# Kernel tuning notes

Measured on AMD Instinct MI355X. Metric: run time of the kernel, lower is better.

The kernel has to match this reference:

```python
import jax, jax.numpy as jnp
import numpy as np

B, T, C = 4, 1024, 2048
H, HKV, HD = 32, 8, 64
HID = 5632  # round_up(8*2048/3, 256)
EPS = 1e-6


def rmsnorm(x, scale):
    return x * scale * jax.lax.rsqrt(jnp.mean(x * x, axis=-1, keepdims=True) + EPS)


def rotary(t, cos, sin):
    # interleaved even/odd rotation, matching torch apply_rotary_emb
    te, to = t[..., ::2], t[..., 1::2]
    return jnp.stack((te * cos - to * sin, te * sin + to * cos), axis=-1).reshape(t.shape)


def setup_inputs() -> dict:
    key = jax.random.key(0)
    ks = jax.random.split(key, 8)
    s = 0.02
    inv = 1.0 / (10000.0 ** (np.arange(0, HD, 2, dtype=np.float64) / HD))
    ang = np.arange(T, dtype=np.float64)[:, None] * inv[None, :]
    return {
        "x": jax.random.normal(ks[0], (B, T, C), jnp.float32),
        "cos": jnp.asarray(np.cos(ang), jnp.float32),
        "sin": jnp.asarray(np.sin(ang), jnp.float32),
        "w_attn": jax.random.normal(ks[1], (C, (H + 2 * HKV) * HD), jnp.float32) * s,
        "w_proj": jax.random.normal(ks[2], (C, C), jnp.float32) * s,
        "w_gate": jax.random.normal(ks[3], (C, HID), jnp.float32) * s,
        "w_up": jax.random.normal(ks[4], (C, HID), jnp.float32) * s,
        "w_down": jax.random.normal(ks[5], (HID, C), jnp.float32) * s,
        "scale1": jnp.ones((C,), jnp.float32),
        "scale2": jnp.ones((C,), jnp.float32),
    }


def reference(x, cos, sin, w_attn, w_proj, w_gate, w_up, w_down, scale1, scale2):
    n_rep = H // HKV
    # --- attention block ---
    h = rmsnorm(x, scale1)
    qkv = h @ w_attn  # [B,T,(H+2*HKV)*HD]
    q, k, v = jnp.split(qkv, [H * HD, (H + HKV) * HD], axis=-1)
    q = q.reshape(B, T, H, HD).transpose(0, 2, 1, 3)      # [B,H,T,HD]
    k = k.reshape(B, T, HKV, HD).transpose(0, 2, 1, 3)    # [B,HKV,T,HD]
    v = v.reshape(B, T, HKV, HD).transpose(0, 2, 1, 3)
    q = rotary(q, cos, sin)
    k = rotary(k, cos, sin)
    # GQA: group q heads over kv heads instead of repeat_interleave
    qg = q.reshape(B, HKV, n_rep, T, HD)
    scores = jnp.einsum('bgrtd,bgsd->bgrts', qg, k) / jnp.sqrt(jnp.float32(HD))
    causal = jnp.tril(jnp.ones((T, T), bool))
    scores = jnp.where(causal, scores, jnp.finfo(scores.dtype).min)
    p = jax.nn.softmax(scores, axis=-1)
    y = jnp.einsum('bgrts,bgsd->bgrtd', p, v)
    y = y.reshape(B, H, T, HD).transpose(0, 2, 1, 3).reshape(B, T, C)
    x = x + y @ w_proj
    # --- SwiGLU MLP block ---
    h2 = rmsnorm(x, scale2)
    x = x + (jax.nn.silu(h2 @ w_gate) * (h2 @ w_up)) @ w_down
    return x
```

## Files before the change

### kernel.cpp

```cpp
#include <hip/hip_runtime.h>
#include <stdint.h>

#define B_ 4
#define T_ 1024
#define C_ 2048
#define H_ 32
#define HKV_ 8
#define HD_ 64
#define HID_ 5632

typedef __attribute__((ext_vector_type(8))) short short8;
typedef __attribute__((ext_vector_type(4))) float floatx4;

__device__ __forceinline__ float b2f(short s) {
  unsigned u = ((unsigned)(unsigned short)s) << 16;
  return __uint_as_float(u);
}
__device__ __forceinline__ short f2b(float f) {
  unsigned u = __float_as_uint(f);
  u = u + 0x7fffu + ((u >> 16) & 1u);
  return (short)(u >> 16);
}
__device__ __forceinline__ unsigned pk2(float a, float b) {
  return ((unsigned)(unsigned short)f2b(a)) |
         ((unsigned)(unsigned short)f2b(b) << 16);
}

#define GL2LDS(gp, lp)                                              \
  __builtin_amdgcn_global_load_lds(                                 \
      (const __attribute__((address_space(1))) void*)(gp),          \
      (__attribute__((address_space(3))) void*)(lp), 16, 0, 0)

__global__ __launch_bounds__(256) void convt_kernel(
    const float* __restrict__ W, short* __restrict__ Wt, int K, int N) {
  __shared__ unsigned u[32][65];
  int n0 = blockIdx.x * 64, k0 = blockIdx.y * 64;
  int tx = threadIdx.x & 63, ty = threadIdx.x >> 6;
#pragma unroll
  for (int j = 0; j < 8; ++j) {
    int kpair = ty * 8 + j;
    float lo = W[(size_t)(k0 + 2 * kpair) * N + n0 + tx];
    float hi = W[(size_t)(k0 + 2 * kpair + 1) * N + n0 + tx];
    u[kpair][tx] = pk2(lo, hi);
  }
  __syncthreads();
  int ny = threadIdx.x >> 2, kx = threadIdx.x & 3;
  unsigned vals[8];
#pragma unroll
  for (int i = 0; i < 8; ++i) vals[i] = u[kx * 8 + i][ny];
  uint4* dst = (uint4*)(Wt + (size_t)(n0 + ny) * K + k0 + kx * 16);
  dst[0] = make_uint4(vals[0], vals[1], vals[2], vals[3]);
  dst[1] = make_uint4(vals[4], vals[5], vals[6], vals[7]);
}

__global__ __launch_bounds__(256) void vt_kernel(
    const short* __restrict__ vin, short* __restrict__ vout) {
  __shared__ short t[32][33];
  int t0 = blockIdx.x * 32, d0 = blockIdx.y * 32, bg = blockIdx.z;
  int tx = threadIdx.x & 31, ty = threadIdx.x >> 5;
  const short* src = vin + (size_t)bg * T_ * HD_;
  short* dst = vout + (size_t)bg * T_ * HD_;
#pragma unroll
  for (int j = 0; j < 4; ++j)
    t[ty + j * 8][tx] = src[(size_t)(t0 + ty + j * 8) * HD_ + d0 + tx];
  __syncthreads();
#pragma unroll
  for (int j = 0; j < 4; ++j)
    dst[(size_t)(d0 + ty + j * 8) * T_ + t0 + tx] = t[tx][ty + j * 8];
}

__global__ __launch_bounds__(256) void rmsnorm_kernel(
    const float* __restrict__ x, const float* __restrict__ scale,
    short* __restrict__ out) {
  int row = blockIdx.x, tid = threadIdx.x;
  const float4* xr = (const float4*)(x + (size_t)row * C_);
  float4 v0 = xr[tid], v1 = xr[tid + 256];
  float s = v0.x * v0.x + v0.y * v0.y + v0.z * v0.z + v0.w * v0.w +
            v1.x * v1.x + v1.y * v1.y + v1.z * v1.z + v1.w * v1.w;
  for (int off = 32; off > 0; off >>= 1) s += __shfl_down(s, off, 64);
  __shared__ float red[4];
  if ((tid & 63) == 0) red[tid >> 6] = s;
  __syncthreads();
  float tot = red[0] + red[1] + red[2] + red[3];
  float r = rsqrtf(tot * (1.0f / (float)C_) + 1e-6f);
  const float4* sc = (const float4*)scale;
  float4 s0 = sc[tid], s1 = sc[tid + 256];
  short* o = out + (size_t)row * C_;
  o[tid * 4 + 0] = f2b(v0.x * s0.x * r);
  o[tid * 4 + 1] = f2b(v0.y * s0.y * r);
  o[tid * 4 + 2] = f2b(v0.z * s0.z * r);
  o[tid * 4 + 3] = f2b(v0.w * s0.w * r);
  o[1024 + tid * 4 + 0] = f2b(v1.x * s1.x * r);
  o[1024 + tid * 4 + 1] = f2b(v1.y * s1.y * r);
  o[1024 + tid * 4 + 2] = f2b(v1.z * s1.z * r);
  o[1024 + tid * 4 + 3] = f2b(v1.w * s1.w * r);
}

template <int EPI>
__global__ __launch_bounds__(256, 2) void gemm128_kernel(
    const short* __restrict__ A, const short* __restrict__ Bt,
    void* __restrict__ Out, const float* __restrict__ resid,
    int M, int N, int K) {
  __shared__ __align__(16) short smem[16384];
  short* As = smem;
  short* Bs = smem + 8192;
  int tid = threadIdx.x, lane = tid & 63, wave = tid >> 6;
  int quad = lane >> 4, l16 = lane & 15;
  int m0 = blockIdx.y * 128, n0 = blockIdx.x * 128;
  int wm = (wave & 1) * 64, wn = (wave >> 1) * 64;

  const short* ap[4];
  const short* bp[4];
  short* lA[4];
  short* lB[4];
#pragma unroll
  for (int c = 0; c < 4; ++c) {
    int S = wave * 256 + c * 64 + lane;
    int row = S >> 3, kc = ((S & 7) - (row & 7)) & 7;
    ap[c] = A + (size_t)(m0 + row) * K + kc * 8;
    bp[c] = Bt + (size_t)(n0 + row) * K + kc * 8;
    lA[c] = As + (wave * 256 + c * 64) * 8;
    lB[c] = Bs + (wave * 256 + c * 64) * 8;
  }

  int aoff[4], boff[4];
#pragma unroll
  for (int i = 0; i < 4; ++i) {
    int ra = wm + i * 16 + l16;
    aoff[i] = (ra * 8 + ((quad + ra) & 7)) * 8;
    int rb = wn + i * 16 + l16;
    boff[i] = (rb * 8 + ((quad + rb) & 7)) * 8;
  }

  floatx4 acc[4][4] = {};
  for (int k0 = 0; k0 < K; k0 += 64) {
#pragma unroll
    for (int c = 0; c < 4; ++c) {
      GL2LDS(ap[c] + k0, lA[c]);
      GL2LDS(bp[c] + k0, lB[c]);
    }
    __syncthreads();
#pragma unroll
    for (int h = 0; h < 2; ++h) {
      short8 af[4], bf[4];
#pragma unroll
      for (int i = 0; i < 4; ++i) af[i] = *(const short8*)(As + (aoff[i] ^ (h * 32)));
#pragma unroll
      for (int i = 0; i < 4; ++i) bf[i] = *(const short8*)(Bs + (boff[i] ^ (h * 32)));
#pragma unroll
      for (int mi = 0; mi < 4; ++mi)
#pragma unroll
        for (int ni = 0; ni < 4; ++ni)
          acc[mi][ni] = __builtin_amdgcn_mfma_f32_16x16x32_bf16(
              af[mi], bf[ni], acc[mi][ni], 0, 0, 0);
    }
    __syncthreads();
  }
#pragma unroll
  for (int mi = 0; mi < 4; ++mi)
#pragma unroll
    for (int ni = 0; ni < 4; ++ni)
#pragma unroll
      for (int r = 0; r < 4; ++r) {
        int row = m0 + wm + mi * 16 + quad * 4 + r;
        int col = n0 + wn + ni * 16 + l16;
        size_t idx = (size_t)row * N + col;
        float a = acc[mi][ni][r];
        if constexpr (EPI == 0)
          ((short*)Out)[idx] = f2b(a);
        else
          ((float*)Out)[idx] = resid[idx] + a;
      }
}

__global__ __launch_bounds__(256, 2) void gateup_kernel(
    const short* __restrict__ A, const short* __restrict__ Wg,
    const short* __restrict__ Wu, short* __restrict__ act, int K) {
  __shared__ __align__(16) short smem[16384];
  short* As = smem;
  short* Bs = smem + 8192;
  int tid = threadIdx.x, lane = tid & 63, wave = tid >> 6;
  int quad = lane >> 4, l16 = lane & 15;
  int m0 = blockIdx.y * 128, n0 = blockIdx.x * 64;
  int wm = (wave & 1) * 64, half = wave >> 1;
  int half_stage = wave >> 1;

  const short* ap[4];
  const short* bp[4];
  short* lA[4];
  short* lB[4];
  const short* Bsel = half_stage ? Wu : Wg;
#pragma unroll
  for (int c = 0; c < 4; ++c) {
    int S = wave * 256 + c * 64 + lane;
    int row = S >> 3, kc = ((S & 7) - (row & 7)) & 7;
    ap[c] = A + (size_t)(m0 + row) * K + kc * 8;
    bp[c] = Bsel + (size_t)(n0 + row - half_stage * 64) * K + kc * 8;
    lA[c] = As + (wave * 256 + c * 64) * 8;
    lB[c] = Bs + (wave * 256 + c * 64) * 8;
  }

  int aoff[4], boff[4];
#pragma unroll
  for (int i = 0; i < 4; ++i) {
    int ra = wm + i * 16 + l16;
    aoff[i] = (ra * 8 + ((quad + ra) & 7)) * 8;
    int rb = half * 64 + i * 16 + l16;
    boff[i] = (rb * 8 + ((quad + rb) & 7)) * 8;
  }

  floatx4 acc[4][4] = {};
  for (int k0 = 0; k0 < K; k0 += 64) {
#pragma unroll
    for (int c = 0; c < 4; ++c) {
      GL2LDS(ap[c] + k0, lA[c]);
      GL2LDS(bp[c] + k0, lB[c]);
    }
    __syncthreads();
#pragma unroll
    for (int h = 0; h < 2; ++h) {
      short8 af[4], bf[4];
#pragma unroll
      for (int i = 0; i < 4; ++i) af[i] = *(const short8*)(As + (aoff[i] ^ (h * 32)));
#pragma unroll
      for (int i = 0; i < 4; ++i) bf[i] = *(const short8*)(Bs + (boff[i] ^ (h * 32)));
#pragma unroll
      for (int mi = 0; mi < 4; ++mi)
#pragma unroll
        for (int ni = 0; ni < 4; ++ni)
          acc[mi][ni] = __builtin_amdgcn_mfma_f32_16x16x32_bf16(
              af[mi], bf[ni], acc[mi][ni], 0, 0, 0);
    }
    __syncthreads();
  }
  short* Ex = smem;
  if (half == 1) {
#pragma unroll
    for (int mi = 0; mi < 4; ++mi)
#pragma unroll
      for (int ni = 0; ni < 4; ++ni)
#pragma unroll
        for (int r = 0; r < 4; ++r)
          Ex[(wm + mi * 16 + quad * 4 + r) * 64 + ni * 16 + l16] =
              f2b(acc[mi][ni][r]);
  }
  __syncthreads();
  if (half == 0) {
#pragma unroll
    for (int mi = 0; mi < 4; ++mi)
#pragma unroll
      for (int ni = 0; ni < 4; ++ni)
#pragma unroll
        for (int r = 0; r < 4; ++r) {
          int row = wm + mi * 16 + quad * 4 + r;
          int col = ni * 16 + l16;
          float u = b2f(Ex[row * 64 + col]);
          float g = acc[mi][ni][r];
          float a = g / (1.0f + __expf(-g)) * u;
          act[(size_t)(m0 + row) * HID_ + n0 + col] = f2b(a);
        }
  }
}

__global__ __launch_bounds__(256) void rope_kernel(
    const short* __restrict__ qkv, const float* __restrict__ cosp,
    const float* __restrict__ sinp, short* __restrict__ q,
    short* __restrict__ k, short* __restrict__ v) {
  int idx = blockIdx.x * 256 + threadIdx.x;
  int i = idx & 31;
  int rest = idx >> 5;
  int head = rest % 48;
  int rest2 = rest / 48;
  int t = rest2 & 1023;
  int b = rest2 >> 10;
  const short* src = qkv + (size_t)(b * T_ + t) * 3072 + head * 64 + 2 * i;
  float e = b2f(src[0]), o = b2f(src[1]);
  if (head < 32) {
    float c = cosp[t * 32 + i], s = sinp[t * 32 + i];
    short* dst = q + ((size_t)(b * 32 + head) * 1024 + t) * 64 + 2 * i;
    dst[0] = f2b((e * c - o * s) * 0.125f);
    dst[1] = f2b((e * s + o * c) * 0.125f);
  } else if (head < 40) {
    float c = cosp[t * 32 + i], s = sinp[t * 32 + i];
    short* dst = k + ((size_t)(b * 8 + (head - 32)) * 1024 + t) * 64 + 2 * i;
    dst[0] = f2b(e * c - o * s);
    dst[1] = f2b(e * s + o * c);
  } else {
    short* dst = v + ((size_t)(b * 8 + (head - 40)) * 1024 + t) * 64 + 2 * i;
    dst[0] = src[0];
    dst[1] = src[1];
  }
}

__global__ __launch_bounds__(256) void attn_kernel(
    const short* __restrict__ q, const short* __restrict__ k,
    const short* __restrict__ vt, short* __restrict__ y) {
  __shared__ __align__(16) short P[4][1024];
  int bx = blockIdx.x, h = blockIdx.y, b = blockIdx.z;
  int lane = threadIdx.x & 63, wave = threadIdx.x >> 6;
  int quad = lane >> 4, l16 = lane & 15;
  int g = h >> 2;
  const short* qp = q + (size_t)(b * H_ + h) * T_ * HD_;
  const short* kp = k + (size_t)(b * HKV_ + g) * T_ * HD_;
  const short* vp = vt + (size_t)(b * HKV_ + g) * T_ * HD_;
  short* Pw = &P[wave][0];
  int sw = (l16 & 7) << 1;
#pragma unroll 1
  for (int half = 0; half < 2; ++half) {
    int tb = half ? (15 - bx) : bx;
    int q0w = tb * 64 + wave * 16;
    int qidx = q0w + l16;
    short8 qf0 = *(const short8*)(qp + (size_t)(q0w + l16) * HD_ + quad * 8);
    short8 qf1 = *(const short8*)(qp + (size_t)(q0w + l16) * HD_ + 32 + quad * 8);
    floatx4 acc[4] = {};
    float m = -1e30f, l = 0.f;
    for (int k0 = 0; k0 <= q0w; k0 += 64) {
      floatx4 st[4];
#pragma unroll
      for (int kt = 0; kt < 4; ++kt) {
        floatx4 z = {0.f, 0.f, 0.f, 0.f};
        const short* kb = kp + (size_t)(k0 + kt * 16 + l16) * HD_;
        short8 kf0 = *(const short8*)(kb + quad * 8);
        short8 kf1 = *(const short8*)(kb + 32 + quad * 8);
        z = __builtin_amdgcn_mfma_f32_16x16x32_bf16(kf0, qf0, z, 0, 0, 0);
        z = __builtin_amdgcn_mfma_f32_16x16x32_bf16(kf1, qf1, z, 0, 0, 0);
        st[kt] = z;
      }
      if (k0 + 64 > q0w) {
#pragma unroll
        for (int kt = 0; kt < 4; ++kt)
#pragma unroll
          for (int r = 0; r < 4; ++r)
            if (k0 + kt * 16 + quad * 4 + r > qidx) st[kt][r] = -1e30f;
      }
      float mloc = -1e30f;
#pragma unroll
      for (int kt = 0; kt < 4; ++kt)
#pragma unroll
        for (int r = 0; r < 4; ++r) mloc = fmaxf(mloc, st[kt][r]);
      mloc = fmaxf(mloc, __shfl_xor(mloc, 16, 64));
      mloc = fmaxf(mloc, __shfl_xor(mloc, 32, 64));
      float mn = fmaxf(m, mloc);
      float alpha = __expf(m - mn);
      m = mn;
      float rsum = 0.f;
#pragma unroll
      for (int kt = 0; kt < 4; ++kt)
#pragma unroll
        for (int r = 0; r < 4; ++r) {
          float p = __expf(st[kt][r] - mn);
          st[kt][r] = p;
          rsum += p;
        }
      rsum += __shfl_xor(rsum, 16, 64);
      rsum += __shfl_xor(rsum, 32, 64);
      l = l * alpha + rsum;
#pragma unroll
      for (int mt = 0; mt < 4; ++mt)
#pragma unroll
        for (int r = 0; r < 4; ++r) acc[mt][r] *= alpha;
#pragma unroll
      for (int kt = 0; kt < 4; ++kt) {
        int hc = (kt * 4 + quad) ^ sw;
        *(uint2*)(Pw + l16 * 64 + hc * 4) =
            make_uint2(pk2(st[kt][0], st[kt][1]), pk2(st[kt][2], st[kt][3]));
      }
#pragma unroll
      for (int chunk = 0; chunk < 2; ++chunk) {
        int hc = (chunk * 8 + quad * 2) ^ sw;
        short8 pf = *(const short8*)(Pw + l16 * 64 + hc * 4);
#pragma unroll
        for (int mt = 0; mt < 4; ++mt) {
          short8 vf = *(const short8*)(vp + (size_t)(mt * 16 + l16) * T_ +
                                       k0 + chunk * 32 + quad * 8);
          acc[mt] =
              __builtin_amdgcn_mfma_f32_16x16x32_bf16(vf, pf, acc[mt], 0, 0, 0);
        }
      }
    }
    float inv = 1.0f / l;
#pragma unroll
    for (int mt = 0; mt < 4; ++mt) {
      int hc = (mt * 4 + quad) ^ sw;
      *(uint2*)(Pw + l16 * 64 + hc * 4) =
          make_uint2(pk2(acc[mt][0] * inv, acc[mt][1] * inv),
                     pk2(acc[mt][2] * inv, acc[mt][3] * inv));
    }
    uint2 o0 = *(uint2*)(Pw + l16 * 64 + (((quad * 4 + 0) ^ sw) * 4));
    uint2 o1 = *(uint2*)(Pw + l16 * 64 + (((quad * 4 + 1) ^ sw) * 4));
    uint2 o2 = *(uint2*)(Pw + l16 * 64 + (((quad * 4 + 2) ^ sw) * 4));
    uint2 o3 = *(uint2*)(Pw + l16 * 64 + (((quad * 4 + 3) ^ sw) * 4));
    uint4* dst =
        (uint4*)(y + (size_t)(b * T_ + q0w + l16) * C_ + h * 64 + quad * 16);
    dst[0] = make_uint4(o0.x, o0.y, o1.x, o1.y);
    dst[1] = make_uint4(o2.x, o2.y, o3.x, o3.y);
  }
}

extern "C" void kernel_launch(void* const* d_in, const int* in_sizes, int n_in,
                              void* d_out, int out_size, void* d_ws, size_t ws_size,
                              hipStream_t stream) {
  const float* x = (const float*)d_in[0];
  const float* cosp = (const float*)d_in[1];
  const float* sinp = (const float*)d_in[2];
  const float* w_attn = (const float*)d_in[3];
  const float* w_proj = (const float*)d_in[4];
  const float* w_gate = (const float*)d_in[5];
  const float* w_up = (const float*)d_in[6];
  const float* w_down = (const float*)d_in[7];
  const float* scale1 = (const float*)d_in[8];
  const float* scale2 = (const float*)d_in[9];
  float* out = (float*)d_out;
  char* ws = (char*)d_ws;

  short* S1 = (short*)(ws + 0);
  short* S2 = (short*)(ws + 23068672);
  short* hbuf = (short*)(ws + 46137344);
  short* S0 = (short*)(ws + 62914560);
  short* qkv = (short*)(ws + 75497472);
  short* kbuf = (short*)(ws + 100663296);
  short* vbuf = (short*)(ws + 104857600);
  short* vtbuf = (short*)(ws + 109051904);
  short* act = (short*)(ws + 62914560);

  convt_kernel<<<dim3(3072 / 64, 2048 / 64), 256, 0, stream>>>(w_attn, S0, 2048, 3072);
  rmsnorm_kernel<<<4096, 256, 0, stream>>>(x, scale1, hbuf);
  gemm128_kernel<0><<<dim3(3072 / 128, 4096 / 128), 256, 0, stream>>>(
      hbuf, S0, qkv, nullptr, 4096, 3072, 2048);
  rope_kernel<<<24576, 256, 0, stream>>>(qkv, cosp, sinp, hbuf, kbuf, vbuf);
  vt_kernel<<<dim3(32, 2, 32), 256, 0, stream>>>(vbuf, vtbuf);
  attn_kernel<<<dim3(8, 32, 4), 256, 0, stream>>>(hbuf, kbuf, vtbuf, qkv);
  convt_kernel<<<dim3(2048 / 64, 2048 / 64), 256, 0, stream>>>(w_proj, S0, 2048, 2048);
  gemm128_kernel<1><<<dim3(2048 / 128, 4096 / 128), 256, 0, stream>>>(
      qkv, S0, out, x, 4096, 2048, 2048);
  rmsnorm_kernel<<<4096, 256, 0, stream>>>(out, scale2, hbuf);
  convt_kernel<<<dim3(5632 / 64, 2048 / 64), 256, 0, stream>>>(w_gate, S1, 2048, 5632);
  convt_kernel<<<dim3(5632 / 64, 2048 / 64), 256, 0, stream>>>(w_up, S2, 2048, 5632);
  gateup_kernel<<<dim3(5632 / 64, 4096 / 128), 256, 0, stream>>>(hbuf, S1, S2, act, 2048);
  convt_kernel<<<dim3(2048 / 64, 5632 / 64), 256, 0, stream>>>(w_down, S1, 5632, 2048);
  gemm128_kernel<1><<<dim3(2048 / 128, 4096 / 128), 256, 0, stream>>>(
      act, S1, out, out, 4096, 2048, 5632);
}
```

Before: 748.3 us.

## Rewrite gate/up GEMM as 256x256 double-buffered tile with interleaved prefetch

```diff
diff --git a/kernel.cpp b/kernel.cpp
--- a/kernel.cpp
+++ b/kernel.cpp
@@ -173,93 +173,197 @@
       }
 }
 
-__global__ __launch_bounds__(256, 2) void gateup_kernel(
+__global__ __launch_bounds__(512, 2) void gateup256_kernel(
     const short* __restrict__ A, const short* __restrict__ Wg,
     const short* __restrict__ Wu, short* __restrict__ act, int K) {
-  __shared__ __align__(16) short smem[16384];
-  short* As = smem;
-  short* Bs = smem + 8192;
+  __shared__ __align__(16) short smem[65536];
+  const int NT = K >> 6;
   int tid = threadIdx.x, lane = tid & 63, wave = tid >> 6;
   int quad = lane >> 4, l16 = lane & 15;
-  int m0 = blockIdx.y * 128, n0 = blockIdx.x * 64;
-  int wm = (wave & 1) * 64, half = wave >> 1;
-  int half_stage = wave >> 1;
-
-  const short* ap[4];
-  const short* bp[4];
-  short* lA[4];
-  short* lB[4];
-  const short* Bsel = half_stage ? Wu : Wg;
-#pragma unroll
-  for (int c = 0; c < 4; ++c) {
-    int S = wave * 256 + c * 64 + lane;
-    int row = S >> 3, kc = ((S & 7) - (row & 7)) & 7;
-    ap[c] = A + (size_t)(m0 + row) * K + kc * 8;
-    bp[c] = Bsel + (size_t)(n0 + row - half_stage * 64) * K + kc * 8;
-    lA[c] = As + (wave * 256 + c * 64) * 8;
-    lB[c] = Bs + (wave * 256 + c * 64) * 8;
-  }
-
-  int aoff[4], boff[4];
+  int wr = wave >> 2, wc = wave & 3;
+  int m0 = blockIdx.y * 256, n0 = blockIdx.x * 128;
+
+  const short* srcp[4][2];
+  int ldsoff[4][2];
+#pragma unroll
+  for (int u = 0; u < 4; ++u)
+#pragma unroll
+    for (int j = 0; j < 2; ++j) {
+      int g = j * 512 + wave * 64 + lane;
+      int c = g & 7, rrel = g >> 3;
+      int R;
+      const short* base;
+      if (u < 2) {
+        R = (rrel & 63) + (rrel >> 6) * 128 + u * 64;
+        base = A + (size_t)(m0 + R) * K;
+      } else {
+        R = (rrel & 31) + (rrel >> 5) * 64 + (u - 2) * 32;
+        base = (R < 128) ? Wg + (size_t)(n0 + R) * K
+                         : Wu + (size_t)(n0 + R - 128) * K;
+      }
+      int kc = (c - (R & 7)) & 7;
+      srcp[u][j] = base + kc * 8;
+      int rr0 = (j * 512 + wave * 64) >> 3;
+      int R0 = (u < 2) ? (rr0 & 63) + (rr0 >> 6) * 128 + u * 64
+                       : (rr0 & 31) + (rr0 >> 5) * 64 + (u - 2) * 32;
+      ldsoff[u][j] = (u < 2 ? 0 : 16384) + R0 * 64;
+    }
+
+#define STG(u, j, par, kt) GL2LDS(srcp[u][j] + (kt), smem + (par)*32768 + ldsoff[u][j])
+#define BAR()                           \
+  {                                     \
+    asm volatile("" ::: "memory");      \
+    __builtin_amdgcn_s_barrier();       \
+    asm volatile("" ::: "memory");      \
+  }
+#define LGK0()                                          \
+  {                                                     \
+    asm volatile("s_waitcnt lgkmcnt(0)" ::: "memory");  \
+    __builtin_amdgcn_sched_barrier(0);                  \
+  }
+
+  int aoff8[8], boff[4];
+#pragma unroll
+  for (int i = 0; i < 8; ++i) {
+    int ra = wr * 128 + i * 16 + l16;
+    aoff8[i] = (ra * 8 + ((quad + ra) & 7)) * 8;
+  }
 #pragma unroll
   for (int i = 0; i < 4; ++i) {
-    int ra = wm + i * 16 + l16;
-    aoff[i] = (ra * 8 + ((quad + ra) & 7)) * 8;
-    int rb = half * 64 + i * 16 + l16;
-    boff[i] = (rb * 8 + ((quad + rb) & 7)) * 8;
-  }
-
-  floatx4 acc[4][4] = {};
-  for (int k0 = 0; k0 < K; k0 += 64) {
-#pragma unroll
-    for (int c = 0; c < 4; ++c) {
-      GL2LDS(ap[c] + k0, lA[c]);
-      GL2LDS(bp[c] + k0, lB[c]);
-    }
-    __syncthreads();
-#pragma unroll
-    for (int h = 0; h < 2; ++h) {
-      short8 af[4], bf[4];
-#pragma unroll
-      for (int i = 0; i < 4; ++i) af[i] = *(const short8*)(As + (aoff[i] ^ (h * 32)));
-#pragma unroll
-      for (int i = 0; i < 4; ++i) bf[i] = *(const short8*)(Bs + (boff[i] ^ (h * 32)));
-#pragma unroll
-      for (int mi = 0; mi < 4; ++mi)
-#pragma unroll
-        for (int ni = 0; ni < 4; ++ni)
-          acc[mi][ni] = __builtin_amdgcn_mfma_f32_16x16x32_bf16(
-              af[mi], bf[ni], acc[mi][ni], 0, 0, 0);
-    }
-    __syncthreads();
-  }
-  short* Ex = smem;
-  if (half == 1) {
-#pragma unroll
-    for (int mi = 0; mi < 4; ++mi)
+    int rb = wc * 64 + i * 16 + l16;
+    boff[i] = 16384 + (rb * 8 + ((quad + rb) & 7)) * 8;
+  }
+
+  floatx4 acc[8][4] = {};
+  short8 a[4][2], b[4][2];
+
+#define RDA(MB, PAR)                                                       \
+  {                                                                        \
+    _Pragma("unroll") for (int i = 0; i < 4; ++i)                          \
+        _Pragma("unroll") for (int h = 0; h < 2; ++h) a[i][h] =            \
+        *(const short8*)(smem + (PAR)*32768 + (aoff8[MB + i] ^ (h * 32))); \
+  }
+#define RDB(NB, PAR)                                                       \
+  {                                                                        \
+    _Pragma("unroll") for (int i = 0; i < 2; ++i)                          \
+        _Pragma("unroll") for (int h = 0; h < 2; ++h) b[NB + i][h] =       \
+        *(const short8*)(smem + (PAR)*32768 + (boff[NB + i] ^ (h * 32)));  \
+  }
+#define MMA(MB, NB)                                                         \
+  {                                                                         \
+    __builtin_amdgcn_s_setprio(1);                                          \
+    _Pragma("unroll") for (int mi = 0; mi < 4; ++mi)                        \
+        _Pragma("unroll") for (int ni = 0; ni < 2; ++ni)                    \
+        _Pragma("unroll") for (int h = 0; h < 2; ++h) acc[MB + mi][NB + ni] = \
+        __builtin_amdgcn_mfma_f32_16x16x32_bf16(                            \
+            a[mi][h], b[NB + ni][h], acc[MB + mi][NB + ni], 0, 0, 0);       \
+    __builtin_amdgcn_s_setprio(0);                                          \
+  }
+
+#pragma unroll
+  for (int u = 0; u < 4; ++u) {
+    STG(u, 0, 0, 0);
+    STG(u, 1, 0, 0);
+  }
+  STG(0, 0, 1, 64); STG(0, 1, 1, 64);
+  STG(2, 0, 1, 64); STG(2, 1, 1, 64);
+  STG(3, 0, 1, 64); STG(3, 1, 1, 64);
+  asm volatile("s_waitcnt vmcnt(6)" ::: "memory");
+  __builtin_amdgcn_sched_barrier(0);
+  BAR();
+
+#pragma unroll 1
+  for (int t = 0; t < NT; t += 2) {
+    int kt1 = (t + 1) << 6, kt2 = (t + 2) << 6, kt3 = (t + 3) << 6;
+    bool pf = (t + 2 < NT);
+    RDA(0, 0); RDB(0, 0);
+    STG(1, 0, 1, kt1); STG(1, 1, 1, kt1);
+    BAR(); LGK0();
+    MMA(0, 0);
+    BAR();
+    RDB(2, 0);
+    if (pf) { STG(0, 0, 0, kt2); STG(0, 1, 0, kt2); }
+    BAR(); LGK0();
+    MMA(0, 2);
+    BAR();
+    RDA(4, 0);
+    if (pf) { STG(2, 0, 0, kt2); STG(2, 1, 0, kt2); }
+    BAR(); LGK0();
+    MMA(4, 0);
+    BAR();
+    if (pf) { STG(3, 0, 0, kt2); STG(3, 1, 0, kt2); }
+    BAR();
+    MMA(4, 2);
+    if (pf) {
+      asm volatile("s_waitcnt vmcnt(6)" ::: "memory");
+    } else {
+      asm volatile("s_waitcnt vmcnt(0)" ::: "memory");
+    }
+    __builtin_amdgcn_sched_barrier(0);
+    BAR();
+    RDA(0, 1); RDB(0, 1);
+    if (pf) { STG(1, 0, 0, kt2); STG(1, 1, 0, kt2); }
+    BAR(); LGK0();
+    MMA(0, 0);
+    BAR();
+    RDB(2, 1);
+    if (pf) { STG(0, 0, 1, kt3); STG(0, 1, 1, kt3); }
+    BAR(); LGK0();
+    MMA(0, 2);
+    BAR();
+    RDA(4, 1);
+    if (pf) { STG(2, 0, 1, kt3); STG(2, 1, 1, kt3); }
+    BAR(); LGK0();
+    MMA(4, 0);
+    BAR();
+    if (pf) { STG(3, 0, 1, kt3); STG(3, 1, 1, kt3); }
+    BAR();
+    MMA(4, 2);
+    if (pf) {
+      asm volatile("s_waitcnt vmcnt(6)" ::: "memory");
+      __builtin_amdgcn_sched_barrier(0);
+    }
+    BAR();
+  }
+
+  asm volatile("s_waitcnt vmcnt(0)" ::: "memory");
+  __syncthreads();
+  if (wc >= 2) {
+    int exb = (wr * 2 + (wc - 2)) * 8192;
+#pragma unroll
+    for (int mi = 0; mi < 8; ++mi)
 #pragma unroll
       for (int ni = 0; ni < 4; ++ni)
-#pragma unroll
-        for (int r = 0; r < 4; ++r)
-          Ex[(wm + mi * 16 + quad * 4 + r) * 64 + ni * 16 + l16] =
-              f2b(acc[mi][ni][r]);
+        *(uint2*)(smem + exb + (ni * 16 + l16) * 128 + mi * 16 + quad * 4) =
+            make_uint2(pk2(acc[mi][ni][0], acc[mi][ni][1]),
+                       pk2(acc[mi][ni][2], acc[mi][ni][3]));
   }
   __syncthreads();
-  if (half == 0) {
-#pragma unroll
-    for (int mi = 0; mi < 4; ++mi)
-#pragma unroll
-      for (int ni = 0; ni < 4; ++ni)
+  if (wc < 2) {
+    int exb = (wr * 2 + wc) * 8192;
+#pragma unroll
+    for (int mi = 0; mi < 8; ++mi)
+#pragma unroll
+      for (int ni = 0; ni < 4; ++ni) {
+        uint2 uv = *(const uint2*)(smem + exb + (ni * 16 + l16) * 128 +
+                                   mi * 16 + quad * 4);
+        float uu[4] = {b2f((short)(uv.x & 0xffff)), b2f((short)(uv.x >> 16)),
+                       b2f((short)(uv.y & 0xffff)), b2f((short)(uv.y >> 16))};
 #pragma unroll
         for (int r = 0; r < 4; ++r) {
-          int row = wm + mi * 16 + quad * 4 + r;
-          int col = ni * 16 + l16;
-          float u = b2f(Ex[row * 64 + col]);
           float g = acc[mi][ni][r];
-          float a = g / (1.0f + __expf(-g)) * u;
-          act[(size_t)(m0 + row) * HID_ + n0 + col] = f2b(a);
+          float v = g / (1.0f + __expf(-g)) * uu[r];
+          act[(size_t)(m0 + wr * 128 + mi * 16 + quad * 4 + r) * HID_ +
+              n0 + wc * 64 + ni * 16 + l16] = f2b(v);
         }
-  }
+      }
+  }
+#undef STG
+#undef BAR
+#undef LGK0
+#undef RDA
+#undef RDB
+#undef MMA
 }
 
 __global__ __launch_bounds__(256) void rope_kernel(
@@ -436,7 +540,8 @@
   rmsnorm_kernel<<<4096, 256, 0, stream>>>(out, scale2, hbuf);
   convt_kernel<<<dim3(5632 / 64, 2048 / 64), 256, 0, stream>>>(w_gate, S1, 2048, 5632);
   convt_kernel<<<dim3(5632 / 64, 2048 / 64), 256, 0, stream>>>(w_up, S2, 2048, 5632);
-  gateup_kernel<<<dim3(5632 / 64, 4096 / 128), 256, 0, stream>>>(hbuf, S1, S2, act, 2048);
+  gateup256_kernel<<<dim3(5632 / 128, 4096 / 256), 512, 0, stream>>>(
+      hbuf, S1, S2, act, 2048);
   convt_kernel<<<dim3(2048 / 64, 5632 / 64), 256, 0, stream>>>(w_down, S1, 5632, 2048);
   gemm128_kernel<1><<<dim3(2048 / 128, 4096 / 128), 256, 0, stream>>>(
       act, S1, out, out, 4096, 2048, 5632);
```

After: 797.8 us. 1.07x slower.
